# Performance work log

Measured on AMD Instinct MI355X. Metric: run time of the kernel, lower is better.

Reference implementation:

```python
import jax, jax.numpy as jnp
import numpy as np

B, T, C = 2, 2048, 2048
N_HEAD = 16

def setup_inputs() -> dict:
    key = jax.random.key(0)
    k1, k2, k3 = jax.random.split(key, 3)
    scale = 1.0 / np.sqrt(C)
    return {
        "x": jax.random.normal(k1, (B, T, C), dtype=jnp.float32),
        "w_attn": jax.random.normal(k2, (C, 3 * C), dtype=jnp.float32) * scale,
        "b_attn": jnp.zeros((3 * C,), dtype=jnp.float32),
        "w_proj": jax.random.normal(k3, (C, C), dtype=jnp.float32) * scale,
        "b_proj": jnp.zeros((C,), dtype=jnp.float32),
    }

def reference(x, w_attn, b_attn, w_proj, b_proj):
    Bb, Tt, Cc = x.shape
    hd = Cc // N_HEAD  # head_size
    qkv = x @ w_attn + b_attn              # [B,T,3C]
    q, k, v = jnp.split(qkv, 3, axis=-1)
    # [B,T,C] -> [B,H,T,hd]
    def heads(t):
        return t.reshape(Bb, Tt, N_HEAD, hd).transpose(0, 2, 1, 3)
    q, k, v = heads(q), heads(k), heads(v)
    att = jnp.einsum("bhqd,bhkd->bhqk", q, k) * (hd ** -0.5)
    causal = jnp.tril(jnp.ones((Tt, Tt), dtype=bool))
    att = jnp.where(causal[None, None], att, -jnp.inf)
    att = jax.nn.softmax(att, axis=-1)
    out = jnp.einsum("bhqk,bhkd->bhqd", att, v)
    out = out.transpose(0, 2, 1, 3).reshape(Bb, Tt, Cc)
    return out @ w_proj + b_proj
```

## Files before the change

kernel.cpp:

```cpp
#include <hip/hip_runtime.h>
#include <cstdint>
#include <cstddef>

typedef __bf16 bf16_t;
typedef __bf16 bf16x8 __attribute__((ext_vector_type(8)));
typedef __bf16 bf16x4 __attribute__((ext_vector_type(4)));
typedef float floatx4 __attribute__((ext_vector_type(4)));

#define B_  2
#define T_  2048
#define C_  2048
#define H_  16
#define HD_ 128

#define K_ATTN_SCALE (0.08838834764831843f * 1.44269504088896f)

__device__ __forceinline__ void async_copy16(const void* g, void* l) {
  __builtin_amdgcn_global_load_lds((const __attribute__((address_space(1))) unsigned int*)g,
                                   (__attribute__((address_space(3))) unsigned int*)l,
                                   16, 0, 0);
}

#define BAR()     asm volatile("s_barrier" ::: "memory")
#define VMCNT(n)  asm volatile("s_waitcnt vmcnt(" #n ")" ::: "memory")

__global__ __launch_bounds__(256) void cvt_f32_bf16(const float* __restrict__ in,
                                                    bf16_t* __restrict__ out, int n4) {
  int i = blockIdx.x * 256 + threadIdx.x;
  if (i >= n4) return;
  const float4 v = ((const float4*)in)[i];
  bf16x4 o;
  o[0] = (bf16_t)v.x; o[1] = (bf16_t)v.y; o[2] = (bf16_t)v.z; o[3] = (bf16_t)v.w;
  ((bf16x4*)out)[i] = o;
}

__global__ __launch_bounds__(256) void transpose_cvt(const float* __restrict__ W,
                                                     bf16_t* __restrict__ Wt,
                                                     int Kd, int Nd) {
  __shared__ float tile[32][33];
  const int tx = threadIdx.x, ty = threadIdx.y;
  const int n0 = blockIdx.x * 32, k0 = blockIdx.y * 32;
#pragma unroll
  for (int j = ty; j < 32; j += 8)
    tile[j][tx] = W[(size_t)(k0 + j) * Nd + n0 + tx];
  __syncthreads();
#pragma unroll
  for (int j = ty; j < 32; j += 8)
    Wt[(size_t)(n0 + j) * Kd + k0 + tx] = (bf16_t)tile[tx][j];
}

#define GBM 256
#define GBN 256
#define GBK 64

__global__ __launch_bounds__(512, 2) void gemm_qkv(
    const bf16_t* __restrict__ A, const bf16_t* __restrict__ Bt,
    const float* __restrict__ bias,
    bf16_t* __restrict__ Qo, bf16_t* __restrict__ Ko, bf16_t* __restrict__ Vo,
    int K) {
  __shared__ __align__(16) char smem[131072];
  const int tid = threadIdx.x;
  const int wave = tid >> 6, lane = tid & 63;
  const int quad = lane >> 4, l15 = lane & 15;
  const int wm = wave >> 2, wn = wave & 3;
  const int bm = blockIdx.y * GBM, bn = blockIdx.x * GBN;

  const bf16_t* asrc[2];
  const bf16_t* bsrc[2];
#pragma unroll
  for (int l = 0; l < 2; ++l) {
    int p = l * 8192 + tid * 16;
    int r = p >> 6;
    int c = ((p >> 4) & 3) ^ ((r >> 1) & 3);
    asrc[l] = A  + (size_t)(bm + r) * K + c * 8;
    bsrc[l] = Bt + (size_t)(bn + r) * K + c * 8;
  }

  auto stage = [&](int buf, int ks, int kofs) {
    char* Asl = smem + buf * 65536 + ks * 16384;
    char* Bsl = Asl + 32768;
#pragma unroll
    for (int l = 0; l < 2; ++l)
      async_copy16(asrc[l] + kofs, Asl + l * 8192 + tid * 16);
#pragma unroll
    for (int l = 0; l < 2; ++l)
      async_copy16(bsrc[l] + kofs, Bsl + l * 8192 + tid * 16);
  };

  const int sxr = ((l15 >> 1) & 3) << 4;
  const int cb  = (quad * 16) ^ sxr;
  const int arow = (wm * 128 + l15) * 64;
  const int brow = (wn * 64 + l15) * 64;

  floatx4 acc[8][4] = {};
  bf16x8 a0[4], a1[4], b0[4], b1[4];

  stage(0, 0, 0);
  stage(0, 1, 32);
  stage(1, 0, GBK);
  VMCNT(8);
  BAR();
  {
    const char* Ab = smem;
    const char* Bb = smem + 32768;
#pragma unroll
    for (int i = 0; i < 4; ++i)
      a0[i] = *(const bf16x8*)(Ab + arow + i * 1024 + cb);
#pragma unroll
    for (int j = 0; j < 4; ++j)
      b0[j] = *(const bf16x8*)(Bb + brow + j * 1024 + cb);
  }

  const int NT = K / GBK;
  for (int t = 0; t < NT; ++t) {
    const char* Ab  = smem + (t & 1) * 65536;
    const char* Bb  = Ab + 32768;
    const char* Abn = smem + ((t + 1) & 1) * 65536;
    const char* Bbn = Abn + 32768;

#pragma unroll
    for (int i = 0; i < 4; ++i)
      a1[i] = *(const bf16x8*)(Ab + arow + 4096 + i * 1024 + cb);
    if (t + 1 < NT) stage((t + 1) & 1, 1, (t + 1) * GBK + 32);
#pragma unroll
    for (int i = 0; i < 4; ++i)
#pragma unroll
      for (int j = 0; j < 4; ++j)
        acc[i][j] = __builtin_amdgcn_mfma_f32_16x16x32_bf16(a0[i], b0[j], acc[i][j], 0, 0, 0);
    if (t + 1 < NT) { VMCNT(8); } else { VMCNT(0); }
    BAR();

#pragma unroll
    for (int i = 0; i < 4; ++i)
      a0[i] = *(const bf16x8*)(Ab + 16384 + arow + i * 1024 + cb);
#pragma unroll
    for (int j = 0; j < 4; ++j)
      b1[j] = *(const bf16x8*)(Bb + 16384 + brow + j * 1024 + cb);
#pragma unroll
    for (int i = 0; i < 4; ++i)
#pragma unroll
      for (int j = 0; j < 4; ++j)
        acc[4 + i][j] = __builtin_amdgcn_mfma_f32_16x16x32_bf16(a1[i], b0[j], acc[4 + i][j], 0, 0, 0);

#pragma unroll
    for (int i = 0; i < 4; ++i)
      a1[i] = *(const bf16x8*)(Ab + 16384 + arow + 4096 + i * 1024 + cb);
    if (t + 2 < NT) stage(t & 1, 0, (t + 2) * GBK);
#pragma unroll
    for (int i = 0; i < 4; ++i)
#pragma unroll
      for (int j = 0; j < 4; ++j)
        acc[i][j] = __builtin_amdgcn_mfma_f32_16x16x32_bf16(a0[i], b1[j], acc[i][j], 0, 0, 0);
    if (t + 2 < NT)      { VMCNT(8); }
    else if (t + 1 < NT) { VMCNT(4); }
    else                 { VMCNT(0); }
    BAR();

    if (t + 1 < NT) {
#pragma unroll
      for (int i = 0; i < 4; ++i)
        a0[i] = *(const bf16x8*)(Abn + arow + i * 1024 + cb);
#pragma unroll
      for (int j = 0; j < 4; ++j)
        b0[j] = *(const bf16x8*)(Bbn + brow + j * 1024 + cb);
    }
#pragma unroll
    for (int i = 0; i < 4; ++i)
#pragma unroll
      for (int j = 0; j < 4; ++j)
        acc[4 + i][j] = __builtin_amdgcn_mfma_f32_16x16x32_bf16(a1[i], b1[j], acc[4 + i][j], 0, 0, 0);
  }

  float bias_r[4];
#pragma unroll
  for (int j = 0; j < 4; ++j)
    bias_r[j] = bias[bn + wn * 64 + j * 16 + l15];

  if (bn < 2 * C_) {
    const int which = bn >> 11;
    bf16_t* dst0 = which ? Ko : Qo;
    const float scl = which ? 1.0f : K_ATTN_SCALE;
#pragma unroll
    for (int i = 0; i < 8; ++i) {
      const int m = bm + wm * 128 + i * 16 + quad * 4;
      const int b = m >> 11, tq = m & 2047;
#pragma unroll
      for (int j = 0; j < 4; ++j) {
        const int n = bn + wn * 64 + j * 16 + l15;
        const int cc = n & 2047;
        const int h = cc >> 7, d = cc & 127;
        bf16_t* dst = dst0 + (((size_t)(b * H_ + h)) * T_ + tq) * HD_ + d;
#pragma unroll
        for (int r = 0; r < 4; ++r)
          dst[(size_t)r * HD_] = (bf16_t)((acc[i][j][r] + bias_r[j]) * scl);
      }
    }
  } else {
    __syncthreads();
    bf16_t* vt = (bf16_t*)smem;
#pragma unroll
    for (int i = 0; i < 8; ++i) {
      const int tl = wm * 128 + i * 16 + quad * 4;
#pragma unroll
      for (int j = 0; j < 4; ++j) {
        const int dl = wn * 64 + j * 16 + l15;
        const int sw = 8 * (dl & 15);
#pragma unroll
        for (int r = 0; r < 4; ++r)
          vt[dl * 256 + ((tl + r) ^ sw)] = (bf16_t)(acc[i][j][r] + bias_r[j]);
      }
    }
    __syncthreads();
    const int dr = tid >> 1, half = tid & 1;
    const int h = ((bn - 2 * C_) >> 7) + (dr >> 7);
    const int b = bm >> 11, t0g = bm & 2047;
    bf16_t* dst = Vo + ((size_t)(b * H_ + h) * HD_ + (dr & 127)) * T_ + t0g;
#pragma unroll
    for (int cc2 = 0; cc2 < 16; ++cc2) {
      const int c = half * 16 + cc2;
      uint4 v = *(const uint4*)&vt[dr * 256 + ((c ^ (dr & 15)) * 8)];
      *(uint4*)(dst + c * 8) = v;
    }
  }
}

#define TM 128
#define TN 128
#define BK 64

__global__ __launch_bounds__(256) void gemm_proj(
    const bf16_t* __restrict__ A, const bf16_t* __restrict__ Bt,
    const float* __restrict__ bias, float* __restrict__ Cout,
    int M, int N, int K) {
  __shared__ __align__(16) char smem[32768];
  bf16_t (*As)[BK] = (bf16_t(*)[BK])smem;
  bf16_t (*Bs)[BK] = (bf16_t(*)[BK])(smem + 16384);
  const int tid = threadIdx.x;
  const int wave = tid >> 6, lane = tid & 63;
  const int quad = lane >> 4, l15 = lane & 15;
  const int bm = blockIdx.y * TM, bn = blockIdx.x * TN;
  const int wm = (wave >> 1) * 64, wn = (wave & 1) * 64;
  const int sw = l15 & 7;

  floatx4 acc[4][4] = {};

  for (int k0 = 0; k0 < K; k0 += BK) {
#pragma unroll
    for (int it = 0; it < 4; ++it) {
      int p = it * 4096 + tid * 16;
      int r = p >> 7;
      int cg = ((p >> 4) & 7) ^ (r & 7);
      async_copy16(A + (size_t)(bm + r) * K + k0 + cg * 8, (char*)&As[0][0] + p);
      async_copy16(Bt + (size_t)(bn + r) * K + k0 + cg * 8, (char*)&Bs[0][0] + p);
    }
    __syncthreads();
#pragma unroll
    for (int kc = 0; kc < 2; ++kc) {
      const int cidx = (kc * 4 + quad) ^ sw;
      bf16x8 af[4], bf[4];
#pragma unroll
      for (int i = 0; i < 4; ++i)
        af[i] = *(const bf16x8*)&As[wm + i * 16 + l15][cidx * 8];
#pragma unroll
      for (int j = 0; j < 4; ++j)
        bf[j] = *(const bf16x8*)&Bs[wn + j * 16 + l15][cidx * 8];
#pragma unroll
      for (int i = 0; i < 4; ++i)
#pragma unroll
        for (int j = 0; j < 4; ++j)
          acc[i][j] = __builtin_amdgcn_mfma_f32_16x16x32_bf16(af[i], bf[j], acc[i][j], 0, 0, 0);
    }
    __syncthreads();
  }

#pragma unroll
  for (int i = 0; i < 4; ++i) {
#pragma unroll
    for (int j = 0; j < 4; ++j) {
#pragma unroll
      for (int r = 0; r < 4; ++r) {
        int m = bm + wm + i * 16 + quad * 4 + r;
        int n = bn + wn + j * 16 + l15;
        Cout[(size_t)m * N + n] = acc[i][j][r] + bias[n];
      }
    }
  }
}

__global__ __launch_bounds__(256) void attn(const bf16_t* __restrict__ Q,
                                            const bf16_t* __restrict__ Kg,
                                            const bf16_t* __restrict__ Vt,
                                            bf16_t* __restrict__ O) {
  __shared__ bf16_t Ks[2][64][128];
  __shared__ bf16_t Vs[2][128][64];
  const int tid = threadIdx.x;
  const int wave = tid >> 6, lane = tid & 63;
  const int quad = lane >> 4, l15 = lane & 15;
  const int j = blockIdx.x;
  const int bh = blockIdx.y;
  const int b = bh >> 4, h = bh & 15;
  const int qtA = 31 - j, qtB = j;
  const int nchA = qtA + 1, nchB = qtB + 1;
  const int q0A = qtA * 64 + wave * 16;
  const int q0B = qtB * 64 + wave * 16;

  const bf16_t* Qh = Q + (size_t)bh * T_ * HD_;
  const bf16_t* Kh = Kg + (size_t)bh * T_ * HD_;
  const bf16_t* Vh = Vt + (size_t)bh * HD_ * T_;

  bf16x8 qfA[4], qfB[4];
#pragma unroll
  for (int kk = 0; kk < 4; ++kk) {
    qfA[kk] = *(const bf16x8*)(Qh + (size_t)(q0A + l15) * HD_ + kk * 32 + quad * 8);
    qfB[kk] = *(const bf16x8*)(Qh + (size_t)(q0B + l15) * HD_ + kk * 32 + quad * 8);
  }

  floatx4 oaccA[8] = {}, oaccB[8] = {};
  float l_A = 0.0f, l_B = 0.0f;

  union PU { bf16x4 v; long long u; };
  union PF { long long u[2]; bf16x8 v; };
  const int lo = ((lane & 16) << 1) + l15;

  auto stage = [&](int buf, int kt0) {
#pragma unroll
    for (int it = 0; it < 4; ++it) {
      int p = it * 4096 + tid * 16;
      int r = p >> 8;
      int cg = ((p >> 4) & 15) ^ (r & 15);
      async_copy16(Kh + (size_t)(kt0 + r) * HD_ + cg * 8, (char*)&Ks[buf][0][0] + p);
    }
#pragma unroll
    for (int it = 0; it < 4; ++it) {
      int p = it * 4096 + tid * 16;
      int r = p >> 7;
      int cg = ((p >> 4) & 7) ^ (r & 7);
      async_copy16(Vh + (size_t)r * T_ + kt0 + cg * 8, (char*)&Vs[buf][0][0] + p);
    }
  };

  auto step = [&](int buf, const bf16x8* qf, floatx4* oacc, float& l_i, int q0, int kt0,
                  bool mask) {
    floatx4 s[4] = {{}, {}, {}, {}};
#pragma unroll
    for (int st = 0; st < 4; ++st) {
#pragma unroll
      for (int kk = 0; kk < 4; ++kk) {
        bf16x8 kf = *(const bf16x8*)&Ks[buf][st * 16 + l15][(((kk * 4 + quad) ^ l15) & 15) * 8];
        s[st] = __builtin_amdgcn_mfma_f32_16x16x32_bf16(kf, qf[kk], s[st], 0, 0, 0);
      }
    }
    float ps = 0.0f;
    long long pu[4];
#pragma unroll
    for (int st = 0; st < 4; ++st) {
      PU t;
#pragma unroll
      for (int r = 0; r < 4; ++r) {
        float val = s[st][r];
        if (mask) {
          int kt = kt0 + st * 16 + quad * 4 + r;
          val = (kt <= q0 + l15) ? val : -3.0e38f;
        }
        float p = exp2f(val);
        ps += p;
        t.v[r] = (bf16_t)p;
      }
      pu[st] = t.u;
    }
    ps += __shfl_xor(ps, 16);
    ps += __shfl_xor(ps, 32);
    l_i += ps;
#pragma unroll
    for (int bb = 0; bb < 2; ++bb) {
      long long lo0 = __shfl(pu[2 * bb], lo);
      long long hi0 = __shfl(pu[2 * bb], lo + 16);
      long long lo1 = __shfl(pu[2 * bb + 1], lo);
      long long hi1 = __shfl(pu[2 * bb + 1], lo + 16);
      PF pf;
      pf.u[0] = (quad >= 2) ? lo1 : lo0;
      pf.u[1] = (quad >= 2) ? hi1 : hi0;
#pragma unroll
      for (int dt = 0; dt < 8; ++dt) {
        bf16x8 vf = *(const bf16x8*)&Vs[buf][dt * 16 + l15][(((bb * 4 + quad) ^ l15) & 7) * 8];
        oacc[dt] = __builtin_amdgcn_mfma_f32_16x16x32_bf16(pf.v, vf, oacc[dt], 0, 0, 0);
      }
    }
  };

  stage(0, 0);
  for (int ch = 0; ch < nchA; ++ch) {
    __syncthreads();
    if (ch + 1 < nchA) stage((ch + 1) & 1, (ch + 1) * 64);
    const int kt0 = ch * 64;
    const int buf = ch & 1;
    step(buf, qfA, oaccA, l_A, q0A, kt0, ch == nchA - 1);
    if (ch < nchB) step(buf, qfB, oaccB, l_B, q0B, kt0, ch == nchB - 1);
  }

  float lrA[4], lrB[4];
#pragma unroll
  for (int r = 0; r < 4; ++r) {
    lrA[r] = __shfl(l_A, quad * 4 + r);
    lrB[r] = __shfl(l_B, quad * 4 + r);
  }
#pragma unroll
  for (int dt = 0; dt < 8; ++dt) {
#pragma unroll
    for (int r = 0; r < 4; ++r) {
      int d = dt * 16 + l15;
      int qa = q0A + quad * 4 + r;
      int qb = q0B + quad * 4 + r;
      O[((size_t)(b * T_ + qa)) * C_ + h * HD_ + d] = (bf16_t)(oaccA[dt][r] / lrA[r]);
      O[((size_t)(b * T_ + qb)) * C_ + h * HD_ + d] = (bf16_t)(oaccB[dt][r] / lrB[r]);
    }
  }
}

extern "C" void kernel_launch(void* const* d_in, const int* in_sizes, int n_in,
                              void* d_out, int out_size, void* d_ws, size_t ws_size,
                              hipStream_t stream) {
  const float* x      = (const float*)d_in[0];
  const float* w_attn = (const float*)d_in[1];
  const float* b_attn = (const float*)d_in[2];
  const float* w_proj = (const float*)d_in[3];
  const float* b_proj = (const float*)d_in[4];
  float* out = (float*)d_out;

  char* p = (char*)d_ws;
  bf16_t* xb  = (bf16_t*)p; p += (size_t)4096 * 2048 * 2;
  bf16_t* waT = (bf16_t*)p; p += (size_t)6144 * 2048 * 2;
  bf16_t* wpT = (bf16_t*)p; p += (size_t)2048 * 2048 * 2;
  bf16_t* Qb  = (bf16_t*)p; p += (size_t)32 * 2048 * 128 * 2;
  bf16_t* Kb  = (bf16_t*)p; p += (size_t)32 * 2048 * 128 * 2;
  bf16_t* Vb  = (bf16_t*)p; p += (size_t)32 * 2048 * 128 * 2;
  bf16_t* Ob  = (bf16_t*)p; p += (size_t)4096 * 2048 * 2;

  cvt_f32_bf16<<<8192, 256, 0, stream>>>(x, xb, 2097152);
  transpose_cvt<<<dim3(6144 / 32, 2048 / 32), dim3(32, 8), 0, stream>>>(w_attn, waT, 2048, 6144);
  transpose_cvt<<<dim3(2048 / 32, 2048 / 32), dim3(32, 8), 0, stream>>>(w_proj, wpT, 2048, 2048);

  gemm_qkv<<<dim3(6144 / GBN, 4096 / GBM), 512, 0, stream>>>(
      xb, waT, b_attn, Qb, Kb, Vb, 2048);

  attn<<<dim3(16, 32), 256, 0, stream>>>(Qb, Kb, Vb, Ob);

  gemm_proj<<<dim3(2048 / TN, 4096 / TM), 256, 0, stream>>>(
      Ob, wpT, b_proj, out, 4096, 2048, 2048);
}
```

Measured before the change: 410.6 us.

## Rewrite attention core with 32x32 MFMA and split-KV waves plus LDS combine

Measured after the change: 412.3 us. Within noise of the previous version (+0.4%).

```diff
diff --git a/kernel.cpp b/kernel.cpp
--- a/kernel.cpp
+++ b/kernel.cpp
@@ -6,6 +6,7 @@
 typedef __bf16 bf16x8 __attribute__((ext_vector_type(8)));
 typedef __bf16 bf16x4 __attribute__((ext_vector_type(4)));
 typedef float floatx4 __attribute__((ext_vector_type(4)));
+typedef float f32x16 __attribute__((ext_vector_type(16)));
 
 #define B_  2
 #define T_  2048
@@ -291,36 +292,23 @@
                                             const bf16_t* __restrict__ Kg,
                                             const bf16_t* __restrict__ Vt,
                                             bf16_t* __restrict__ O) {
-  __shared__ bf16_t Ks[2][64][128];
-  __shared__ bf16_t Vs[2][128][64];
+  __shared__ __align__(16) char smem[66560];
   const int tid = threadIdx.x;
   const int wave = tid >> 6, lane = tid & 63;
-  const int quad = lane >> 4, l15 = lane & 15;
+  const int hi = lane >> 5, l31 = lane & 31;
+  const int qh = wave & 1, kh = wave >> 1;
   const int j = blockIdx.x;
   const int bh = blockIdx.y;
   const int b = bh >> 4, h = bh & 15;
   const int qtA = 31 - j, qtB = j;
   const int nchA = qtA + 1, nchB = qtB + 1;
-  const int q0A = qtA * 64 + wave * 16;
-  const int q0B = qtB * 64 + wave * 16;
 
   const bf16_t* Qh = Q + (size_t)bh * T_ * HD_;
   const bf16_t* Kh = Kg + (size_t)bh * T_ * HD_;
   const bf16_t* Vh = Vt + (size_t)bh * HD_ * T_;
 
-  bf16x8 qfA[4], qfB[4];
-#pragma unroll
-  for (int kk = 0; kk < 4; ++kk) {
-    qfA[kk] = *(const bf16x8*)(Qh + (size_t)(q0A + l15) * HD_ + kk * 32 + quad * 8);
-    qfB[kk] = *(const bf16x8*)(Qh + (size_t)(q0B + l15) * HD_ + kk * 32 + quad * 8);
-  }
-
-  floatx4 oaccA[8] = {}, oaccB[8] = {};
-  float l_A = 0.0f, l_B = 0.0f;
-
-  union PU { bf16x4 v; long long u; };
-  union PF { long long u[2]; bf16x8 v; };
-  const int lo = ((lane & 16) << 1) + l15;
+  float* xb32 = (float*)smem;
+  float* lbuf = (float*)(smem + 65536);
 
   auto stage = [&](int buf, int kt0) {
 #pragma unroll
@@ -328,62 +316,84 @@
       int p = it * 4096 + tid * 16;
       int r = p >> 8;
       int cg = ((p >> 4) & 15) ^ (r & 15);
-      async_copy16(Kh + (size_t)(kt0 + r) * HD_ + cg * 8, (char*)&Ks[buf][0][0] + p);
+      async_copy16(Kh + (size_t)(kt0 + r) * HD_ + cg * 8, smem + buf * 16384 + p);
     }
 #pragma unroll
     for (int it = 0; it < 4; ++it) {
       int p = it * 4096 + tid * 16;
       int r = p >> 7;
       int cg = ((p >> 4) & 7) ^ (r & 7);
-      async_copy16(Vh + (size_t)r * T_ + kt0 + cg * 8, (char*)&Vs[buf][0][0] + p);
-    }
-  };
-
-  auto step = [&](int buf, const bf16x8* qf, floatx4* oacc, float& l_i, int q0, int kt0,
-                  bool mask) {
-    floatx4 s[4] = {{}, {}, {}, {}};
-#pragma unroll
-    for (int st = 0; st < 4; ++st) {
-#pragma unroll
-      for (int kk = 0; kk < 4; ++kk) {
-        bf16x8 kf = *(const bf16x8*)&Ks[buf][st * 16 + l15][(((kk * 4 + quad) ^ l15) & 15) * 8];
-        s[st] = __builtin_amdgcn_mfma_f32_16x16x32_bf16(kf, qf[kk], s[st], 0, 0, 0);
-      }
-    }
+      async_copy16(Vh + (size_t)r * T_ + kt0 + cg * 8, smem + 32768 + buf * 16384 + p);
+    }
+  };
+
+  const int q0Arow = qtA * 64 + qh * 32;
+  const int q0Brow = qtB * 64 + qh * 32;
+  const bf16_t* qpA = Qh + (size_t)(q0Arow + l31) * HD_ + hi * 8;
+  const bf16_t* qpB = Qh + (size_t)(q0Brow + l31) * HD_ + hi * 8;
+
+  f32x16 oA[4] = {}, oB[4] = {};
+  float l_A = 0.0f, l_B = 0.0f;
+
+  const int swk = l31 & 15;
+  const int swv = l31 & 7;
+  const int krbase = (kh * 32 + l31) * 256;
+
+  auto slot = [&](int buf, int kt0, const bf16_t* qp, f32x16 (&oacc)[4], float& l_i,
+                  int qrow, bool mask) {
+    const char* Kb = smem + buf * 16384;
+    const char* Vb = smem + 32768 + buf * 16384;
+    f32x16 s0 = {}, s1 = {};
+#pragma unroll
+    for (int m = 0; m < 4; ++m) {
+      bf16x8 kf = *(const bf16x8*)(Kb + krbase + (((2 * m + hi) ^ swk) << 4));
+      bf16x8 qf = *(const bf16x8*)(qp + m * 16);
+      s0 = __builtin_amdgcn_mfma_f32_32x32x16_bf16(kf, qf, s0, 0, 0, 0);
+    }
+#pragma unroll
+    for (int m = 4; m < 8; ++m) {
+      bf16x8 kf = *(const bf16x8*)(Kb + krbase + (((2 * m + hi) ^ swk) << 4));
+      bf16x8 qf = *(const bf16x8*)(qp + m * 16);
+      s1 = __builtin_amdgcn_mfma_f32_32x32x16_bf16(kf, qf, s1, 0, 0, 0);
+    }
+    const int qg = qrow + l31;
+    float p[16];
     float ps = 0.0f;
-    long long pu[4];
-#pragma unroll
-    for (int st = 0; st < 4; ++st) {
-      PU t;
-#pragma unroll
-      for (int r = 0; r < 4; ++r) {
-        float val = s[st][r];
-        if (mask) {
-          int kt = kt0 + st * 16 + quad * 4 + r;
-          val = (kt <= q0 + l15) ? val : -3.0e38f;
-        }
-        float p = exp2f(val);
-        ps += p;
-        t.v[r] = (bf16_t)p;
-      }
-      pu[st] = t.u;
-    }
-    ps += __shfl_xor(ps, 16);
+#pragma unroll
+    for (int r = 0; r < 16; ++r) {
+      float v = s0[r] + s1[r];
+      float e = __builtin_amdgcn_exp2f(v);
+      if (mask) {
+        int kt = kt0 + kh * 32 + (r & 3) + 8 * (r >> 2) + 4 * hi;
+        e = (kt <= qg) ? e : 0.0f;
+      }
+      ps += e;
+      p[r] = e;
+    }
     ps += __shfl_xor(ps, 32);
     l_i += ps;
-#pragma unroll
-    for (int bb = 0; bb < 2; ++bb) {
-      long long lo0 = __shfl(pu[2 * bb], lo);
-      long long hi0 = __shfl(pu[2 * bb], lo + 16);
-      long long lo1 = __shfl(pu[2 * bb + 1], lo);
-      long long hi1 = __shfl(pu[2 * bb + 1], lo + 16);
-      PF pf;
-      pf.u[0] = (quad >= 2) ? lo1 : lo0;
-      pf.u[1] = (quad >= 2) ? hi1 : hi0;
-#pragma unroll
-      for (int dt = 0; dt < 8; ++dt) {
-        bf16x8 vf = *(const bf16x8*)&Vs[buf][dt * 16 + l15][(((bb * 4 + quad) ^ l15) & 7) * 8];
-        oacc[dt] = __builtin_amdgcn_mfma_f32_16x16x32_bf16(pf.v, vf, oacc[dt], 0, 0, 0);
+    union PF { unsigned int w[4]; bf16x8 v; } pf[2];
+#pragma unroll
+    for (int m2 = 0; m2 < 2; ++m2) {
+      union PK { bf16_t h[2]; unsigned int u; } a0, a1, c0, c1;
+      const int ga = 8 * m2, gb = 8 * m2 + 4;
+      a0.h[0] = (bf16_t)p[ga + 0]; a0.h[1] = (bf16_t)p[ga + 1];
+      a1.h[0] = (bf16_t)p[ga + 2]; a1.h[1] = (bf16_t)p[ga + 3];
+      c0.h[0] = (bf16_t)p[gb + 0]; c0.h[1] = (bf16_t)p[gb + 1];
+      c1.h[0] = (bf16_t)p[gb + 2]; c1.h[1] = (bf16_t)p[gb + 3];
+      unsigned int wa0 = a0.u, wa1 = a1.u, wb0 = c0.u, wb1 = c1.u;
+      asm("v_permlane32_swap_b32 %0, %1" : "+v"(wa0), "+v"(wb0));
+      asm("v_permlane32_swap_b32 %0, %1" : "+v"(wa1), "+v"(wb1));
+      pf[m2].w[0] = wa0; pf[m2].w[1] = wa1; pf[m2].w[2] = wb0; pf[m2].w[3] = wb1;
+    }
+#pragma unroll
+    for (int g = 0; g < 4; ++g) {
+      const int vrb = (g * 32 + l31) * 128;
+#pragma unroll
+      for (int m2 = 0; m2 < 2; ++m2) {
+        const int cc = kh * 4 + m2 * 2 + hi;
+        bf16x8 vf = *(const bf16x8*)(Vb + vrb + ((cc ^ swv) << 4));
+        oacc[g] = __builtin_amdgcn_mfma_f32_32x32x16_bf16(vf, pf[m2].v, oacc[g], 0, 0, 0);
       }
     }
   };
@@ -392,29 +402,60 @@
   for (int ch = 0; ch < nchA; ++ch) {
     __syncthreads();
     if (ch + 1 < nchA) stage((ch + 1) & 1, (ch + 1) * 64);
-    const int kt0 = ch * 64;
     const int buf = ch & 1;
-    step(buf, qfA, oaccA, l_A, q0A, kt0, ch == nchA - 1);
-    if (ch < nchB) step(buf, qfB, oaccB, l_B, q0B, kt0, ch == nchB - 1);
-  }
-
-  float lrA[4], lrB[4];
-#pragma unroll
-  for (int r = 0; r < 4; ++r) {
-    lrA[r] = __shfl(l_A, quad * 4 + r);
-    lrB[r] = __shfl(l_B, quad * 4 + r);
-  }
-#pragma unroll
-  for (int dt = 0; dt < 8; ++dt) {
-#pragma unroll
-    for (int r = 0; r < 4; ++r) {
-      int d = dt * 16 + l15;
-      int qa = q0A + quad * 4 + r;
-      int qb = q0B + quad * 4 + r;
-      O[((size_t)(b * T_ + qa)) * C_ + h * HD_ + d] = (bf16_t)(oaccA[dt][r] / lrA[r]);
-      O[((size_t)(b * T_ + qb)) * C_ + h * HD_ + d] = (bf16_t)(oaccB[dt][r] / lrB[r]);
-    }
-  }
+    slot(buf, ch * 64, qpA, oA, l_A, q0Arow, ch == nchA - 1);
+    if (ch < nchB)
+      slot(buf, ch * 64, qpB, oB, l_B, q0Brow, ch == nchB - 1);
+  }
+
+  auto dumpAcc = [&](f32x16 (&o)[4], float lp) {
+#pragma unroll
+    for (int g = 0; g < 4; ++g)
+#pragma unroll
+      for (int r = 0; r < 16; ++r)
+        xb32[qh * 4096 + (g * 16 + r) * 64 + lane] = o[g][r];
+    lbuf[qh * 64 + lane] = lp;
+  };
+  auto combineTile = [&](f32x16 (&o)[4], float lp) {
+    const float inv = 1.0f / (lp + lbuf[qh * 64 + lane]);
+    const int rr = qh * 32 + l31;
+    char* ob = smem + 32768 + rr * 256;
+#pragma unroll
+    for (int g = 0; g < 4; ++g)
+#pragma unroll
+      for (int r1 = 0; r1 < 4; ++r1) {
+        union { bf16_t hh[4]; uint2 u2; } w;
+#pragma unroll
+        for (int k = 0; k < 4; ++k)
+          w.hh[k] = (bf16_t)((o[g][r1 * 4 + k] +
+                              xb32[qh * 4096 + (g * 16 + r1 * 4 + k) * 64 + lane]) * inv);
+        const int chunk = 4 * g + r1;
+        *(uint2*)(ob + ((chunk ^ (rr & 15)) << 4) + 8 * hi) = w.u2;
+      }
+  };
+  auto storeTile = [&](int qt) {
+    const int row = tid >> 2, seg = tid & 3;
+    bf16_t* Og = O + ((size_t)(b * T_ + qt * 64 + row)) * C_ + h * HD_;
+    const char* sb = smem + 32768 + row * 256;
+#pragma unroll
+    for (int c4 = 0; c4 < 4; ++c4) {
+      const int c = seg * 4 + c4;
+      uint4 v = *(const uint4*)(sb + ((c ^ (row & 15)) << 4));
+      *(uint4*)(Og + c * 8) = v;
+    }
+  };
+
+  __syncthreads();
+  if (wave >= 2) dumpAcc(oA, l_A);
+  __syncthreads();
+  if (wave < 2) combineTile(oA, l_A);
+  __syncthreads();
+  storeTile(qtA);
+  if (wave >= 2) dumpAcc(oB, l_B);
+  __syncthreads();
+  if (wave < 2) combineTile(oB, l_B);
+  __syncthreads();
+  storeTile(qtB);
 }
 
 extern "C" void kernel_launch(void* const* d_in, const int* in_sizes, int n_in,
```
